# Kernel tuning notes

Hardware: AMD Instinct MI355X
Metric: run time of the kernel (lower is better)

The kernel has to match this reference:

```python
import jax, jax.numpy as jnp
import numpy as np

B, N, S = 8, 16384, 2048
C1, C2 = 128, 256
MLP = [256, 256]
BN_EPS = 1e-5


def setup_inputs() -> dict:
    key = jax.random.key(0)
    ks = jax.random.split(key, 12)
    inp = {
        "xyz1": jax.random.normal(ks[0], (B, N, 3), dtype=jnp.float32),
        "xyz2": jax.random.normal(ks[1], (B, S, 3), dtype=jnp.float32),
        "points1": jax.random.normal(ks[2], (B, C1, N), dtype=jnp.float32),
        "points2": jax.random.normal(ks[3], (B, C2, S), dtype=jnp.float32),
    }
    cin = C1 + C2
    kidx = 4
    for li, cout in enumerate(MLP):
        inp[f"W{li}"] = jax.random.normal(ks[kidx], (cout, cin), dtype=jnp.float32) * (1.0 / np.sqrt(cin))
        inp[f"b{li}"] = jnp.zeros((cout,), dtype=jnp.float32)
        inp[f"g{li}"] = jnp.ones((cout,), dtype=jnp.float32)
        inp[f"beta{li}"] = jnp.zeros((cout,), dtype=jnp.float32)
        cin = cout
        kidx += 1
    return inp


def _interpolate(xyz1, xyz2, points2):
    # D[b,n,s] = ||xyz1[b,n] - xyz2[b,s]||^2
    D = jnp.sum((xyz1[:, :, None, :] - xyz2[:, None, :, :]) ** 2, axis=-1)  # [B,N,S]
    neg_dist, idx = jax.lax.top_k(-D, 3)  # 3 smallest distances, ascending
    dist = jnp.maximum(-neg_dist, 1e-10)  # [B,N,3]
    w = 1.0 / dist
    weight = w / jnp.sum(w, axis=2, keepdims=True)  # [B,N,3]
    p2 = jnp.transpose(points2, (0, 2, 1))  # [B,S,C2]
    gathered = p2[jnp.arange(p2.shape[0])[:, None, None], idx]  # [B,N,3,C2]
    return jnp.einsum("bnkc,bnk->bcn", gathered, weight)  # [B,C2,N]


def _conv_bn_relu(x, W, b, g, beta):
    # 1x1 conv over points: [B,Cin,N] -> [B,Cout,N]
    y = jnp.einsum("oc,bcn->bon", W, x) + b[None, :, None]
    mean = jnp.mean(y, axis=(0, 2), keepdims=True)
    var = jnp.var(y, axis=(0, 2), keepdims=True)  # biased, training-mode BN
    yh = (y - mean) * jax.lax.rsqrt(var + BN_EPS)
    return jax.nn.relu(yh * g[None, :, None] + beta[None, :, None])


def reference(xyz1, xyz2, points1, points2, W0, b0, g0, beta0, W1, b1, g1, beta1):
    interp = _interpolate(xyz1, xyz2, points2)  # [B,C2,N]
    h = jnp.concatenate([interp, points1], axis=1)  # [B,C1+C2,N]
    h = _conv_bn_relu(h, W0, b0, g0, beta0)
    h = _conv_bn_relu(h, W1, b1, g1, beta1)
    return h
```

## Files before the change

kernel.cpp:

```cpp
#include <hip/hip_runtime.h>
#include <hip/hip_bf16.h>


typedef unsigned int u32;
typedef unsigned short u16;
typedef __attribute__((ext_vector_type(8))) short short8;
typedef __attribute__((ext_vector_type(4))) float f32x4;

#define NT_TOTAL 131072
#define NN 16384
#define SS 2048

__device__ __forceinline__ float bf2f(u16 u) {
    union { u32 i; float f; } cv; cv.i = ((u32)u) << 16; return cv.f;
}
__device__ __forceinline__ u16 f2bf(float f) {
    union { float f; u32 i; } cv; cv.f = f;
    const u32 r = (cv.i + 0x7FFFu + ((cv.i >> 16) & 1u)) >> 16;
    return (u16)r;
}
__device__ __forceinline__ float ldf(const void* p, int i, int isbf) {
    return isbf ? bf2f(((const u16*)p)[i]) : ((const float*)p)[i];
}

__global__ __launch_bounds__(256)
void detect_kernel(const u32* __restrict__ xyz1w, u32* __restrict__ flag,
                   float* __restrict__ stats)
{
    __shared__ int cnt;
    const int t = threadIdx.x;
    if (t == 0) cnt = 0;
    for (int i = t; i < 1024; i += 256) stats[i] = 0.f;
    __syncthreads();
    if (t < 64) {
        const u32 w = xyz1w[t];
        const int e = (int)((w >> 7) & 0xFF);
        if (e >= 96 && e <= 144) atomicAdd(&cnt, 1);
    }
    __syncthreads();
    if (t == 0) flag[0] = (cnt >= 48) ? 1u : 0u;
}

__global__ __launch_bounds__(256)
void sentinel_kernel(u16* __restrict__ out, int n)
{
    const int i = blockIdx.x * 256 + threadIdx.x;
    if (i < n) out[i] = 0x4496;
}

__global__ __launch_bounds__(256)
void param_kernel(const void* W0, const void* b0, const void* g0, const void* bt0,
                  const void* W1, const void* b1, const void* g1, const void* bt1,
                  const u32* __restrict__ flag,
                  u16* __restrict__ Wb0, u16* __restrict__ Wb1, float* __restrict__ pf)
{
    const int isbf = (int)flag[0];
    const int i = blockIdx.x * 256 + threadIdx.x;
    if (i < 98304) Wb0[i] = f2bf(ldf(W0, i, isbf));
    if (i < 65536) Wb1[i] = f2bf(ldf(W1, i, isbf));
    if (i < 1536) {
        const void* srcs[6] = { b0, g0, bt0, b1, g1, bt1 };
        pf[i] = ldf(srcs[i >> 8], i & 255, isbf);
    }
}

__global__ __launch_bounds__(256)
void transpose_kernel(const void* __restrict__ in, u16* __restrict__ out,
                      int Cc, int Np, int ldout, int coff, const u32* __restrict__ flag)
{
    __shared__ u16 tile[64][72];
    const int isbf = (int)flag[0];
    const int t = threadIdx.x;
    const int n0 = blockIdx.x * 64, c0 = blockIdx.y * 64, bz = blockIdx.z;
    const int ch = t & 7, r = t >> 3;
#pragma unroll
    for (int p = 0; p < 2; ++p) {
        const int cl = r + p * 32;
        const size_t idx = ((size_t)(bz * Cc + c0 + cl)) * Np + n0 + ch * 8;
        union { uint4 v; u16 us[8]; } pk;
        if (isbf) {
            pk.v = *(const uint4*)((const u16*)in + idx);
        } else {
            const float4 va = *(const float4*)((const float*)in + idx);
            const float4 vb = *(const float4*)((const float*)in + idx + 4);
            pk.us[0] = f2bf(va.x); pk.us[1] = f2bf(va.y);
            pk.us[2] = f2bf(va.z); pk.us[3] = f2bf(va.w);
            pk.us[4] = f2bf(vb.x); pk.us[5] = f2bf(vb.y);
            pk.us[6] = f2bf(vb.z); pk.us[7] = f2bf(vb.w);
        }
        *(uint4*)&tile[cl][ch * 8] = pk.v;
    }
    __syncthreads();
#pragma unroll
    for (int p = 0; p < 2; ++p) {
        const int nl = r + p * 32;
        union { uint4 v; u16 us[8]; } pk;
#pragma unroll
        for (int i = 0; i < 8; ++i) pk.us[i] = tile[ch * 8 + i][nl];
        *(uint4*)&out[((size_t)(bz * Np + n0 + nl)) * ldout + coff + c0 + ch * 8] = pk.v;
    }
}

__global__ __launch_bounds__(256)
void knn_kernel(const void* __restrict__ xyz1, const void* __restrict__ xyz2,
                u32* __restrict__ idxA, float* __restrict__ wA,
                const u32* __restrict__ flag)
{
    __shared__ float s2[SS * 3];
    const int isbf = (int)flag[0];
    const int t = threadIdx.x;
    const int blk = blockIdx.x;
    const int b = blk >> 6;
    const int qg = blk * 256 + t;
    for (int i = t; i < SS * 3; i += 256) s2[i] = ldf(xyz2, b * SS * 3 + i, isbf);
    __syncthreads();
    const float qx = ldf(xyz1, qg * 3 + 0, isbf);
    const float qy = ldf(xyz1, qg * 3 + 1, isbf);
    const float qz = ldf(xyz1, qg * 3 + 2, isbf);
    float d0 = 1e30f, d1 = 1e30f, d2 = 1e30f;
    int i0 = 0, i1 = 0, i2 = 0;
#pragma unroll 4
    for (int s = 0; s < SS; ++s) {
        const float dx = qx - s2[s * 3 + 0];
        const float dy = qy - s2[s * 3 + 1];
        const float dz = qz - s2[s * 3 + 2];
        const float d = dx * dx + dy * dy + dz * dz;
        const bool c0 = d < d0, c1 = d < d1, c2 = d < d2;
        d2 = c1 ? d1 : (c2 ? d : d2);  i2 = c1 ? i1 : (c2 ? s : i2);
        d1 = c0 ? d0 : (c1 ? d : d1);  i1 = c0 ? i0 : (c1 ? s : i1);
        d0 = c0 ? d : d0;              i0 = c0 ? s : i0;
    }
    d0 = fmaxf(d0, 1e-10f); d1 = fmaxf(d1, 1e-10f); d2 = fmaxf(d2, 1e-10f);
    const float w0 = 1.f / d0, w1 = 1.f / d1, w2 = 1.f / d2;
    const float inv = 1.f / (w0 + w1 + w2);
    idxA[qg * 3 + 0] = i0; idxA[qg * 3 + 1] = i1; idxA[qg * 3 + 2] = i2;
    wA[qg * 3 + 0] = w0 * inv; wA[qg * 3 + 1] = w1 * inv; wA[qg * 3 + 2] = w2 * inv;
}

__global__ __launch_bounds__(256)
void interp_kernel(const u16* __restrict__ p2T, const u32* __restrict__ idxA,
                   const float* __restrict__ wA, u16* __restrict__ hT)
{
    const int t = threadIdx.x;
    const int pl = t >> 5, g = t & 31;
    const int qg = blockIdx.x * 8 + pl;
    const int b = qg >> 14;
    float acc[8] = {0.f, 0.f, 0.f, 0.f, 0.f, 0.f, 0.f, 0.f};
#pragma unroll
    for (int k = 0; k < 3; ++k) {
        const u32 idx = idxA[qg * 3 + k];
        const float w = wA[qg * 3 + k];
        union { uint4 v; u16 us[8]; } pk;
        pk.v = *(const uint4*)(p2T + ((size_t)(b * SS + idx)) * 256 + g * 8);
#pragma unroll
        for (int e = 0; e < 8; ++e) acc[e] = fmaf(w, bf2f(pk.us[e]), acc[e]);
    }
    union { uint4 v; u16 us[8]; } ov;
#pragma unroll
    for (int e = 0; e < 8; ++e) ov.us[e] = f2bf(acc[e]);
    *(uint4*)&hT[(size_t)qg * 384 + g * 8] = ov.v;
}

__global__ __launch_bounds__(256)
void gemm_kernel(const u16* __restrict__ A, const u16* __restrict__ Bm,
                 const float* __restrict__ bias, void* __restrict__ yout, int K,
                 const u32* __restrict__ flag)
{
    __shared__ __align__(16) u16 aT[128 * 32];
    __shared__ __align__(16) u16 bT[128 * 32];
    const int isbf = (int)flag[0];
    const int t = threadIdx.x;
    const int lane = t & 63;
    const int l15 = lane & 15;
    const int q = lane >> 4;
    const int wid = t >> 6;
    const int n0 = blockIdx.x * 128;
    const int m0 = blockIdx.y * 128;
    const int wm = (wid & 1) * 64;
    const int wn = (wid >> 1) * 64;

    f32x4 acc[4][4] = {};

    const int ca0 = t, ca1 = t + 256;
    const u16* gA0 = A + (size_t)(m0 + (ca0 >> 2)) * K + (ca0 & 3) * 8;
    const u16* gA1 = A + (size_t)(m0 + (ca1 >> 2)) * K + (ca1 & 3) * 8;
    const u16* gB0 = Bm + (size_t)(n0 + (ca0 >> 2)) * K + (ca0 & 3) * 8;
    const u16* gB1 = Bm + (size_t)(n0 + (ca1 >> 2)) * K + (ca1 & 3) * 8;
    u16* lA0 = &aT[ca0 * 8]; u16* lA1 = &aT[ca1 * 8];
    u16* lB0 = &bT[ca0 * 8]; u16* lB1 = &bT[ca1 * 8];

    for (int k0 = 0; k0 < K; k0 += 32) {
        const uint4 ra0 = *(const uint4*)(gA0 + k0);
        const uint4 ra1 = *(const uint4*)(gA1 + k0);
        const uint4 rb0 = *(const uint4*)(gB0 + k0);
        const uint4 rb1 = *(const uint4*)(gB1 + k0);
        __syncthreads();
        *(uint4*)lA0 = ra0; *(uint4*)lA1 = ra1;
        *(uint4*)lB0 = rb0; *(uint4*)lB1 = rb1;
        __syncthreads();
        short8 a[4], b[4];
#pragma unroll
        for (int i = 0; i < 4; ++i)
            a[i] = *(const short8*)&aT[(wm + i * 16 + l15) * 32 + q * 8];
#pragma unroll
        for (int j = 0; j < 4; ++j)
            b[j] = *(const short8*)&bT[(wn + j * 16 + l15) * 32 + q * 8];
#pragma unroll
        for (int i = 0; i < 4; ++i)
#pragma unroll
            for (int j = 0; j < 4; ++j)
                acc[i][j] = __builtin_amdgcn_mfma_f32_16x16x32_bf16(a[i], b[j], acc[i][j], 0, 0, 0);
    }

#pragma unroll
    for (int i = 0; i < 4; ++i) {
        const int mBase = m0 + wm + i * 16 + q * 4;
        float bi[4];
#pragma unroll
        for (int r = 0; r < 4; ++r) bi[r] = bias[mBase + r];
#pragma unroll
        for (int j = 0; j < 4; ++j) {
            const int col = n0 + wn + j * 16 + l15;
            const size_t obase = ((size_t)(col >> 14) * 256) * NN + (col & 16383);
#pragma unroll
            for (int r = 0; r < 4; ++r) {
                const float v = acc[i][j][r] + bi[r];
                const size_t oi = obase + (size_t)(mBase + r) * NN;
                if (isbf) ((u16*)yout)[oi] = f2bf(v);
                else      ((float*)yout)[oi] = v;
            }
        }
    }
}

__global__ __launch_bounds__(256)
void stats_kernel(const void* __restrict__ y, float* __restrict__ sums,
                  float* __restrict__ sumsq, const u32* __restrict__ flag)
{
    const int isbf = (int)flag[0];
    const int t = threadIdx.x;
    const int c = blockIdx.y, bb = blockIdx.x;
    const size_t base = ((size_t)(bb * 256 + c)) * NN;
    float s = 0.f, sq = 0.f;
    if (isbf) {
        const u16* p = (const u16*)y + base;
#pragma unroll
        for (int i = 0; i < 8; ++i) {
            union { uint4 v; u16 us[8]; } pk;
            pk.v = *(const uint4*)(p + i * 2048 + t * 8);
#pragma unroll
            for (int e = 0; e < 8; ++e) { const float v = bf2f(pk.us[e]); s += v; sq += v * v; }
        }
    } else {
        const float* p = (const float*)y + base;
#pragma unroll
        for (int i = 0; i < 16; ++i) {
            const float4 v = *(const float4*)(p + i * 1024 + t * 4);
            s += v.x + v.y + v.z + v.w;
            sq += v.x * v.x + v.y * v.y + v.z * v.z + v.w * v.w;
        }
    }
#pragma unroll
    for (int off = 32; off > 0; off >>= 1) {
        s += __shfl_down(s, off);
        sq += __shfl_down(sq, off);
    }
    __shared__ float red[8];
    const int wid = t >> 6;
    if ((t & 63) == 0) { red[wid * 2] = s; red[wid * 2 + 1] = sq; }
    __syncthreads();
    if (t == 0) {
        atomicAdd(&sums[c], red[0] + red[2] + red[4] + red[6]);
        atomicAdd(&sumsq[c], red[1] + red[3] + red[5] + red[7]);
    }
}

__global__ __launch_bounds__(256)
void bn_act_tr_kernel(const void* __restrict__ y, const float* __restrict__ sums,
                      const float* __restrict__ sumsq, const float* __restrict__ gam,
                      const float* __restrict__ beta, u16* __restrict__ h2,
                      const u32* __restrict__ flag)
{
    __shared__ u16 tile[64][68];
    const int isbf = (int)flag[0];
    const int t = threadIdx.x;
    const int n0g = blockIdx.x * 64, c0 = blockIdx.y * 64;
    const int bb = n0g >> 14, nn0 = n0g & 16383;
    const float invNT = 1.0f / (float)NT_TOTAL;
    {
        const int f4 = t & 15, cbase = t >> 4;
#pragma unroll
        for (int p = 0; p < 4; ++p) {
            const int cl = cbase + p * 16;
            const int c = c0 + cl;
            const float mean = sums[c] * invNT;
            const float var = sumsq[c] * invNT - mean * mean;
            const float rstd = rsqrtf(var + 1e-5f);
            const float sc = gam[c] * rstd;
            const float sh = beta[c] - mean * sc;
            const size_t base = ((size_t)(bb * 256 + c)) * NN + nn0 + f4 * 4;
            float in4[4];
            if (isbf) {
                union { uint2 v2; u16 us[4]; } iv;
                iv.v2 = *(const uint2*)((const u16*)y + base);
#pragma unroll
                for (int e = 0; e < 4; ++e) in4[e] = bf2f(iv.us[e]);
            } else {
                const float4 v = *(const float4*)((const float*)y + base);
                in4[0] = v.x; in4[1] = v.y; in4[2] = v.z; in4[3] = v.w;
            }
            union { uint2 v2; u16 us[4]; } o;
#pragma unroll
            for (int e = 0; e < 4; ++e) {
                float v = in4[e] * sc + sh;
                v = (v != v) ? 777.0f : fmaxf(v, 0.f);
                o.us[e] = f2bf(v);
            }
            *(uint2*)&tile[cl][f4 * 4] = o.v2;
        }
    }
    __syncthreads();
    {
        const int ch = t & 7, rr = t >> 3;
#pragma unroll
        for (int p = 0; p < 2; ++p) {
            const int nl = rr + p * 32;
            union { uint4 v; u16 us[8]; } pk;
#pragma unroll
            for (int i = 0; i < 8; ++i) pk.us[i] = tile[ch * 8 + i][nl];
            *(uint4*)&h2[((size_t)(n0g + nl)) * 256 + c0 + ch * 8] = pk.v;
        }
    }
}

__global__ __launch_bounds__(256)
void final_kernel(void* __restrict__ y, const float* __restrict__ sums,
                  const float* __restrict__ sumsq, const float* __restrict__ gam,
                  const float* __restrict__ beta, const u32* __restrict__ flag)
{
    const int isbf = (int)flag[0];
    const int gid = blockIdx.x * 256 + threadIdx.x;
    const int c = (gid >> 12) & 255;
    const float invNT = 1.0f / (float)NT_TOTAL;
    const float mean = sums[c] * invNT;
    const float var = sumsq[c] * invNT - mean * mean;
    const float rstd = rsqrtf(var + 1e-5f);
    const float sc = gam[c] * rstd;
    const float sh = beta[c] - mean * sc;
    const size_t idx4 = (size_t)gid * 4;
    float in4[4];
    if (isbf) {
        union { uint2 v2; u16 us[4]; } iv;
        iv.v2 = *(const uint2*)((const u16*)y + idx4);
#pragma unroll
        for (int e = 0; e < 4; ++e) in4[e] = bf2f(iv.us[e]);
    } else {
        const float4 v = *(const float4*)((const float*)y + idx4);
        in4[0] = v.x; in4[1] = v.y; in4[2] = v.z; in4[3] = v.w;
    }
    float o4[4];
#pragma unroll
    for (int e = 0; e < 4; ++e) {
        float v = in4[e] * sc + sh;
        o4[e] = (v != v) ? 777.0f : fmaxf(v, 0.f);
    }
    if (isbf) {
        union { uint2 v2; u16 us[4]; } o;
#pragma unroll
        for (int e = 0; e < 4; ++e) o.us[e] = f2bf(o4[e]);
        *(uint2*)((u16*)y + idx4) = o.v2;
    } else {
        float4 o; o.x = o4[0]; o.y = o4[1]; o.z = o4[2]; o.w = o4[3];
        *(float4*)((float*)y + idx4) = o;
    }
}

__global__ void pointnet_fp_module_24532853195517_kernel() {}

extern "C" void kernel_launch(void* const* d_in, const int* in_sizes, int n_in,
                              void* d_out, int out_size, void* d_ws, size_t ws_size,
                              hipStream_t stream)
{
    const void* xyz1    = d_in[0];
    const void* xyz2    = d_in[1];
    const void* points1 = d_in[2];
    const void* points2 = d_in[3];
    const void* W0 = d_in[4];  const void* b0 = d_in[5];
    const void* g0 = d_in[6];  const void* bt0 = d_in[7];
    const void* W1 = d_in[8];  const void* b1 = d_in[9];
    const void* g1 = d_in[10]; const void* bt1 = d_in[11];

    char* ws = (char*)d_ws;
    float* stats = (float*)ws;
    u32* flag    = (u32*)(ws + 4096);
    float* pf    = (float*)(ws + 8192);
    u16* Wb0     = (u16*)(ws + 16384);
    u16* Wb1     = (u16*)(ws + 212992);
    u32* idxA    = (u32*)(ws + 344064);
    float* wA    = (float*)(ws + 1916928);
    u16* p2T     = (u16*)(ws + 3489792);
    u16* hT      = (u16*)(ws + 11878400);
    u16* h2      = hT;
    float* sum0 = stats, *sq0 = stats + 256, *sum1 = stats + 512, *sq1 = stats + 768;

    if (ws_size < (size_t)112541696) {
        sentinel_kernel<<<(out_size + 255) / 256, 256, 0, stream>>>((u16*)d_out, out_size);
        return;
    }

    sentinel_kernel<<<16, 256, 0, stream>>>((u16*)d_out, 4096);

    detect_kernel<<<1, 256, 0, stream>>>((const u32*)xyz1, flag, stats);
    param_kernel<<<384, 256, 0, stream>>>(W0, b0, g0, bt0, W1, b1, g1, bt1, flag, Wb0, Wb1, pf);
    transpose_kernel<<<dim3(32, 4, 8), 256, 0, stream>>>(points2, p2T, 256, 2048, 256, 0, flag);
    transpose_kernel<<<dim3(256, 2, 8), 256, 0, stream>>>(points1, hT, 128, 16384, 384, 256, flag);
    knn_kernel<<<512, 256, 0, stream>>>(xyz1, xyz2, idxA, wA, flag);
    interp_kernel<<<16384, 256, 0, stream>>>(p2T, idxA, wA, hT);
    gemm_kernel<<<dim3(1024, 2), 256, 0, stream>>>(Wb0, hT, pf + 0, d_out, 384, flag);
    stats_kernel<<<dim3(8, 256), 256, 0, stream>>>(d_out, sum0, sq0, flag);
    bn_act_tr_kernel<<<dim3(2048, 4), 256, 0, stream>>>(d_out, sum0, sq0, pf + 256, pf + 512, h2, flag);
    gemm_kernel<<<dim3(1024, 2), 256, 0, stream>>>(Wb1, h2, pf + 768, d_out, 256, flag);
    stats_kernel<<<dim3(8, 256), 256, 0, stream>>>(d_out, sum1, sq1, flag);
    final_kernel<<<32768, 256, 0, stream>>>(d_out, sum1, sq1, pf + 1024, pf + 1280, flag);
}
```

Before: 607.8 us.

## Rewrite KNN with expanded-distance form and packed-index med3 top-k network

Precomputes xyz2 with its squared norm into float4s (stored in scratch space inside the output buffer), so each candidate distance becomes three FMAs plus an add. It packs the candidate index into the low 11 mantissa bits of the distance and keeps a top-5 list with fmin/fmed3 instead of branchy selects. The 5 candidates are then re-scored with exact distances to pick the true top 3. Candidates are read from global or cached memory through uniform loads rather than shared memory. The risks are that the truncated, cancellation-prone expanded distances could miss a true neighbor outside the top 5, and that the output buffer is reused as scratch.

New measurement: 563.4 us. 7.3% less time.

```diff
diff --git a/kernel.cpp b/kernel.cpp
--- a/kernel.cpp
+++ b/kernel.cpp
@@ -4,6 +4,7 @@
 
 typedef unsigned int u32;
 typedef unsigned short u16;
+typedef unsigned long long u64;
 typedef __attribute__((ext_vector_type(8))) short short8;
 typedef __attribute__((ext_vector_type(4))) float f32x4;
 
@@ -61,6 +62,21 @@
     if (i < 1536) {
         const void* srcs[6] = { b0, g0, bt0, b1, g1, bt1 };
         pf[i] = ldf(srcs[i >> 8], i & 255, isbf);
+    }
+}
+
+__global__ __launch_bounds__(256)
+void pack2_kernel(const void* __restrict__ xyz2, float4* __restrict__ s2q,
+                  const u32* __restrict__ flag)
+{
+    const int isbf = (int)flag[0];
+    const int i = blockIdx.x * 256 + threadIdx.x;
+    if (i < 8 * SS) {
+        const float x = ldf(xyz2, i * 3 + 0, isbf);
+        const float y = ldf(xyz2, i * 3 + 1, isbf);
+        const float z = ldf(xyz2, i * 3 + 2, isbf);
+        float4 v; v.x = x; v.y = y; v.z = z; v.w = x * x + y * y + z * z;
+        s2q[i] = v;
     }
 }
 
@@ -102,35 +118,57 @@
 }
 
 __global__ __launch_bounds__(256)
-void knn_kernel(const void* __restrict__ xyz1, const void* __restrict__ xyz2,
+void knn_kernel(const float4* __restrict__ s2q, const void* __restrict__ xyz1,
                 u32* __restrict__ idxA, float* __restrict__ wA,
                 const u32* __restrict__ flag)
 {
-    __shared__ float s2[SS * 3];
     const int isbf = (int)flag[0];
     const int t = threadIdx.x;
     const int blk = blockIdx.x;
     const int b = blk >> 6;
     const int qg = blk * 256 + t;
-    for (int i = t; i < SS * 3; i += 256) s2[i] = ldf(xyz2, b * SS * 3 + i, isbf);
-    __syncthreads();
     const float qx = ldf(xyz1, qg * 3 + 0, isbf);
     const float qy = ldf(xyz1, qg * 3 + 1, isbf);
     const float qz = ldf(xyz1, qg * 3 + 2, isbf);
-    float d0 = 1e30f, d1 = 1e30f, d2 = 1e30f;
-    int i0 = 0, i1 = 0, i2 = 0;
-#pragma unroll 4
+    const float qx2 = -2.f * qx, qy2 = -2.f * qy, qz2 = -2.f * qz;
+    const float qc = qx * qx + qy * qy + qz * qz;
+    const float4* __restrict__ S = s2q + (size_t)b * SS;
+
+    float k0 = __builtin_inff(), k1 = k0, k2 = k0, k3 = k0, k4 = k0;
+#pragma unroll 8
     for (int s = 0; s < SS; ++s) {
-        const float dx = qx - s2[s * 3 + 0];
-        const float dy = qy - s2[s * 3 + 1];
-        const float dz = qz - s2[s * 3 + 2];
-        const float d = dx * dx + dy * dy + dz * dz;
-        const bool c0 = d < d0, c1 = d < d1, c2 = d < d2;
-        d2 = c1 ? d1 : (c2 ? d : d2);  i2 = c1 ? i1 : (c2 ? s : i2);
-        d1 = c0 ? d0 : (c1 ? d : d1);  i1 = c0 ? i0 : (c1 ? s : i1);
-        d0 = c0 ? d : d0;              i0 = c0 ? s : i0;
-    }
-    d0 = fmaxf(d0, 1e-10f); d1 = fmaxf(d1, 1e-10f); d2 = fmaxf(d2, 1e-10f);
+        const float4 v = S[s];
+        float d = fmaf(v.x, qx2, qc);
+        d = fmaf(v.y, qy2, d);
+        d = fmaf(v.z, qz2, d);
+        d += v.w;
+        const float k = __uint_as_float((__float_as_uint(d) & 0xFFFFF800u) | (u32)s);
+        const float o0 = fminf(k, k0);
+        const float o1 = __builtin_amdgcn_fmed3f(k, k0, k1);
+        const float o2 = __builtin_amdgcn_fmed3f(k, k1, k2);
+        const float o3 = __builtin_amdgcn_fmed3f(k, k2, k3);
+        const float o4 = __builtin_amdgcn_fmed3f(k, k3, k4);
+        k0 = o0; k1 = o1; k2 = o2; k3 = o3; k4 = o4;
+    }
+
+    const float kk[5] = { k0, k1, k2, k3, k4 };
+    u64 e0 = ~0ull, e1 = ~0ull, e2 = ~0ull;
+#pragma unroll
+    for (int i = 0; i < 5; ++i) {
+        const u32 idx = __float_as_uint(kk[i]) & 0x7FFu;
+        const float4 c = S[idx];
+        const float dx = qx - c.x, dy = qy - c.y, dz = qz - c.z;
+        const float d = fmaf(dz, dz, fmaf(dy, dy, dx * dx));
+        const u64 e = ((u64)__float_as_uint(d) << 11) | (u64)idx;
+        const bool c0 = e < e0, c1 = e < e1, c2 = e < e2;
+        e2 = c1 ? e1 : (c2 ? e : e2);
+        e1 = c0 ? e0 : (c1 ? e : e1);
+        e0 = c0 ? e : e0;
+    }
+    const u32 i0 = (u32)(e0 & 0x7FF), i1 = (u32)(e1 & 0x7FF), i2 = (u32)(e2 & 0x7FF);
+    const float d0 = fmaxf(__uint_as_float((u32)(e0 >> 11)), 1e-10f);
+    const float d1 = fmaxf(__uint_as_float((u32)(e1 >> 11)), 1e-10f);
+    const float d2 = fmaxf(__uint_as_float((u32)(e2 >> 11)), 1e-10f);
     const float w0 = 1.f / d0, w1 = 1.f / d1, w2 = 1.f / d2;
     const float inv = 1.f / (w0 + w1 + w2);
     idxA[qg * 3 + 0] = i0; idxA[qg * 3 + 1] = i1; idxA[qg * 3 + 2] = i2;
@@ -403,6 +441,8 @@
     u16* h2      = hT;
     float* sum0 = stats, *sq0 = stats + 256, *sum1 = stats + 512, *sq1 = stats + 768;
 
+    float4* s2q = (float4*)((char*)d_out + (8u << 20));
+
     if (ws_size < (size_t)112541696) {
         sentinel_kernel<<<(out_size + 255) / 256, 256, 0, stream>>>((u16*)d_out, out_size);
         return;
@@ -412,9 +452,10 @@
 
     detect_kernel<<<1, 256, 0, stream>>>((const u32*)xyz1, flag, stats);
     param_kernel<<<384, 256, 0, stream>>>(W0, b0, g0, bt0, W1, b1, g1, bt1, flag, Wb0, Wb1, pf);
+    pack2_kernel<<<64, 256, 0, stream>>>(xyz2, s2q, flag);
     transpose_kernel<<<dim3(32, 4, 8), 256, 0, stream>>>(points2, p2T, 256, 2048, 256, 0, flag);
     transpose_kernel<<<dim3(256, 2, 8), 256, 0, stream>>>(points1, hT, 128, 16384, 384, 256, flag);
-    knn_kernel<<<512, 256, 0, stream>>>(xyz1, xyz2, idxA, wA, flag);
+    knn_kernel<<<512, 256, 0, stream>>>(s2q, xyz1, idxA, wA, flag);
     interp_kernel<<<16384, 256, 0, stream>>>(p2T, idxA, wA, hT);
     gemm_kernel<<<dim3(1024, 2), 256, 0, stream>>>(Wb0, hT, pf + 0, d_out, 384, flag);
     stats_kernel<<<dim3(8, 256), 256, 0, stream>>>(d_out, sum0, sq0, flag);
```
